# Optimization experiments

Hardware: AMD Instinct MI355X
Metric: run time of the kernel (lower is better)

The kernel has to match this reference:

```python
import jax, jax.numpy as jnp
import numpy as np


def _quantize(x, weight):
    # x: (B, D, H, W); weight: (D, K)
    B, D, H, W = x.shape
    K = weight.shape[1]
    xf = x.reshape(B, D, H * W)  # (B, D, N)
    x2 = jnp.sum(xf * xf, axis=1)                      # (B, N)
    cross = jnp.einsum('bdn,dk->bnk', xf, weight)       # (B, N, K)
    e2 = jnp.sum(weight * weight, axis=0)               # (K,)
    d2 = x2[..., None] - 2.0 * cross + e2               # (B, N, K)
    argmin = jnp.argmin(d2, axis=-1)                    # (B, N)
    # gather codes: (B, N, D) -> (B, D, N) -> (B, D, H, W)
    quant = weight.T[argmin]                            # (B, N, D)
    result = jnp.transpose(quant, (0, 2, 1)).reshape(B, D, H, W)
    return result, argmin.reshape(B, H, W)


def setup_inputs() -> dict:
    key = jax.random.key(0)
    k1, k2 = jax.random.split(key)
    x = jax.random.normal(k1, (32, 256, 32, 32), dtype=jnp.float32)
    weight = jax.random.uniform(k2, (256, 512), dtype=jnp.float32)  # torch.rand init
    return {"x": x, "weight": weight}


def reference(x, weight):
    result, argmin = _quantize(x, weight)
    return result, argmin
```

## Files before the change

### kernel.cpp

```cpp
#include <hip/hip_runtime.h>

typedef __attribute__((ext_vector_type(8))) short bf16x8;
typedef __attribute__((ext_vector_type(16))) float f32x16;

__device__ __forceinline__ bool lex_lt(float av, int ai, float bv, int bi) {
  return av < bv || (av == bv && ai < bi);
}

__device__ __forceinline__ unsigned bf16_rne(float v) {
  unsigned u = __float_as_uint(v);
  return (u + 0x7fffu + ((u >> 16) & 1u)) >> 16;
}

__device__ __forceinline__ unsigned pk_bf16(float a, float b) {
  return bf16_rne(a) | (bf16_rne(b) << 16);
}

__global__ __launch_bounds__(256) void vq_pre(
    const float* __restrict__ w, float* __restrict__ e2,
    short* __restrict__ wtil, float* __restrict__ wT) {
  int blk = blockIdx.x;
  if (blk < 64) {
    int gid = blk * 256 + threadIdx.x;
    int n  = gid & 511;
    int kg = gid >> 9;
    bf16x8 hv, lv;
    float vv[8];
#pragma unroll
    for (int j = 0; j < 8; ++j) {
      float v = w[(kg * 8 + j) * 512 + n];
      vv[j] = v;
      unsigned h = bf16_rne(v);
      float hf = __uint_as_float(h << 16);
      unsigned l = bf16_rne(v - hf);
      hv[j] = (short)h;
      lv[j] = (short)l;
    }
    short* dst = wtil + (size_t)gid * 8;
    *(bf16x8*)dst = hv;
    *(bf16x8*)(dst + 131072) = lv;
    if (wT) {
      float* p = wT + (size_t)n * 256 + kg * 8;
      *(float4*)p       = make_float4(vv[0], vv[1], vv[2], vv[3]);
      *(float4*)(p + 4) = make_float4(vv[4], vv[5], vv[6], vv[7]);
    }
  } else {
    int t = (blk - 64) * 256 + threadIdx.x;
    int k = t >> 2;
    int part = t & 3;
    double s = 0.0;
#pragma unroll 8
    for (int d = part * 64; d < part * 64 + 64; ++d) {
      double v = (double)w[d * 512 + k];
      s = fma(v, v, s);
    }
    s += __shfl_xor(s, 1);
    s += __shfl_xor(s, 2);
    if (part == 0) e2[k] = (float)s;
  }
}

__global__ __launch_bounds__(512, 4) void vq_main(
    const float* __restrict__ x, const float* __restrict__ w,
    const float* __restrict__ e2g, const short* __restrict__ wtil,
    const float* __restrict__ wT,
    float* __restrict__ out, float* __restrict__ arg_out) {
  __shared__ __align__(16) char arena[76800];
  short* xh   = (short*)arena;
  short* xl   = (short*)(arena + 32768);
  float* e2s  = (float*)(arena + 65536);
  float* tv1  = (float*)(arena + 67584);
  float* tv2  = (float*)(arena + 69632);
  int*   ti1  = (int*)(arena + 71680);
  int*   ti2  = (int*)(arena + 73728);
  int*   p1S  = (int*)(arena + 75776);
  int*   p2S  = (int*)(arena + 76032);
  int*   needS= (int*)(arena + 76288);
  int*   rpickS=(int*)(arena + 76544);
  float* gbuf = (float*)arena;

  const int tid = threadIdx.x;
  const int b  = blockIdx.x >> 4;
  const int n0 = (blockIdx.x & 15) << 6;
  const float* xbase = x + (size_t)b * 262144 + n0;

  {
    e2s[tid] = e2g[tid];
    const int n4  = tid & 15;
    const int kgp = tid >> 4;
    float4 v[8];
#pragma unroll
    for (int j = 0; j < 8; ++j)
      v[j] = *(const float4*)(xbase + (size_t)(kgp * 8 + j) * 1024 + (n4 << 2));
#pragma unroll
    for (int i = 0; i < 4; ++i) {
      int m = (n4 << 2) + i;
      union { int w4[4]; bf16x8 v8; } H, L;
#pragma unroll
      for (int jj = 0; jj < 4; ++jj) {
        float a = (i == 0) ? v[2*jj].x : (i == 1) ? v[2*jj].y : (i == 2) ? v[2*jj].z : v[2*jj].w;
        float c = (i == 0) ? v[2*jj+1].x : (i == 1) ? v[2*jj+1].y : (i == 2) ? v[2*jj+1].z : v[2*jj+1].w;
        unsigned hu = pk_bf16(a, c);
        float haf = __uint_as_float(hu << 16);
        float hcf = __uint_as_float(hu & 0xffff0000u);
        unsigned lu = pk_bf16(a - haf, c - hcf);
        H.w4[jj] = (int)hu;
        L.w4[jj] = (int)lu;
      }
      int slot = kgp ^ (m & 7) ^ ((m >> 3) & 7);
      int off = (m << 8) + (slot << 3);
      *(bf16x8*)&xh[off] = H.v8;
      *(bf16x8*)&xl[off] = L.v8;
    }
  }
  __syncthreads();

  const int lane = tid & 63;
  const int wv   = tid >> 6;
  const int ln   = lane & 31;
  const int half = lane >> 5;
  const int wb   = wv << 6;

  f32x16 acc[2][2];
#pragma unroll
  for (int ct = 0; ct < 2; ++ct)
#pragma unroll
    for (int pt = 0; pt < 2; ++pt)
#pragma unroll
      for (int r = 0; r < 16; ++r) acc[ct][pt][r] = 0.f;

  const int asw = (ln & 7) ^ (ln >> 3);
  const int abase = ln << 8;

  int bofs[2];
#pragma unroll
  for (int ct = 0; ct < 2; ++ct) bofs[ct] = (wb + (ct << 5) + ln) << 3;

  bf16x8 pch[2], pcl[2];
#pragma unroll
  for (int ct = 0; ct < 2; ++ct) {
    const short* p = wtil + (half << 12) + bofs[ct];
    pch[ct] = *(const bf16x8*)p;
    pcl[ct] = *(const bf16x8*)(p + 131072);
  }

  auto kstep = [&](int ch) {
    const int kg = (ch << 1) + half;
    const int ao = abase + ((kg ^ asw) << 3);
    bf16x8 xf[2], xg[2];
#pragma unroll
    for (int pt = 0; pt < 2; ++pt) {
      const int ap = (ao + (pt << 13)) ^ (pt << 5);
      xf[pt] = *(const bf16x8*)&xh[ap];
      xg[pt] = *(const bf16x8*)&xl[ap];
    }
    bf16x8 cfh[2], cfl[2];
#pragma unroll
    for (int ct = 0; ct < 2; ++ct) { cfh[ct] = pch[ct]; cfl[ct] = pcl[ct]; }
    if (ch < 15) {
      const int kgn = ((ch + 1) << 1) + half;
#pragma unroll
      for (int ct = 0; ct < 2; ++ct) {
        const short* p = wtil + (kgn << 12) + bofs[ct];
        pch[ct] = *(const bf16x8*)p;
        pcl[ct] = *(const bf16x8*)(p + 131072);
      }
    }
#pragma unroll
    for (int ct = 0; ct < 2; ++ct)
#pragma unroll
      for (int pt = 0; pt < 2; ++pt) {
        acc[ct][pt] = __builtin_amdgcn_mfma_f32_32x32x16_bf16(cfh[ct], xf[pt], acc[ct][pt], 0, 0, 0);
        acc[ct][pt] = __builtin_amdgcn_mfma_f32_32x32x16_bf16(cfh[ct], xg[pt], acc[ct][pt], 0, 0, 0);
        acc[ct][pt] = __builtin_amdgcn_mfma_f32_32x32x16_bf16(cfl[ct], xf[pt], acc[ct][pt], 0, 0, 0);
      }
  };

  kstep(0);  kstep(1);  kstep(2);  kstep(3);
  kstep(4);  kstep(5);  kstep(6);  kstep(7);
  kstep(8);  kstep(9);  kstep(10); kstep(11);
  kstep(12); kstep(13); kstep(14); kstep(15);

  float e2r[2][16];
#pragma unroll
  for (int ct = 0; ct < 2; ++ct)
#pragma unroll
    for (int r = 0; r < 16; ++r)
      e2r[ct][r] = e2s[wb + (ct << 5) + (r & 3) + ((r >> 2) << 3) + (half << 2)];

#pragma unroll
  for (int pt = 0; pt < 2; ++pt) {
    float v1 = 3.4e38f, v2 = 3.4e38f;
    int i1 = 0x7fffffff, i2 = 0x7fffffff;
#pragma unroll
    for (int ct = 0; ct < 2; ++ct) {
#pragma unroll
      for (int r = 0; r < 16; ++r) {
        int k = wb + (ct << 5) + (r & 3) + ((r >> 2) << 3) + (half << 2);
        float s = fmaf(-2.f, acc[ct][pt][r], e2r[ct][r]);
        if (lex_lt(s, k, v1, i1)) { v2 = v1; i2 = i1; v1 = s; i1 = k; }
        else if (lex_lt(s, k, v2, i2)) { v2 = s; i2 = k; }
      }
    }
    {
      float ov1 = __shfl_xor(v1, 32);
      int   oi1 = __shfl_xor(i1, 32);
      float ov2 = __shfl_xor(v2, 32);
      int   oi2 = __shfl_xor(i2, 32);
      bool aFirst = lex_lt(v1, i1, ov1, oi1);
      float nv1 = aFirst ? v1 : ov1;  int ni1 = aFirst ? i1 : oi1;
      float cv  = aFirst ? ov1 : v1;  int ci  = aFirst ? oi1 : i1;
      float sv  = aFirst ? v2 : ov2;  int si  = aFirst ? i2 : oi2;
      bool cFirst = lex_lt(cv, ci, sv, si);
      v1 = nv1; i1 = ni1;
      v2 = cFirst ? cv : sv; i2 = cFirst ? ci : si;
    }
    if (half == 0) {
      int s = (wv << 6) + (pt << 5) + ln;
      tv1[s] = v1; ti1[s] = i1; tv2[s] = v2; ti2[s] = i2;
    }
  }
  __syncthreads();

  if (tid < 64) {
    int row = tid;
    float v1 = 3.4e38f, v2 = 3.4e38f;
    int i1 = 0x7fffffff, i2 = 0x7fffffff;
#pragma unroll
    for (int wvv = 0; wvv < 8; ++wvv) {
      int s = (wvv << 6) + row;
      float a1 = tv1[s]; int ai = ti1[s];
      float a2 = tv2[s]; int bi = ti2[s];
      if (lex_lt(a1, ai, v1, i1)) { v2 = v1; i2 = i1; v1 = a1; i1 = ai; }
      else if (lex_lt(a1, ai, v2, i2)) { v2 = a1; i2 = ai; }
      if (lex_lt(a2, bi, v1, i1)) { v2 = v1; i2 = i1; v1 = a2; i1 = bi; }
      else if (lex_lt(a2, bi, v2, i2)) { v2 = a2; i2 = bi; }
    }
    p1S[row] = i1; p2S[row] = i2;
    needS[row] = (v2 - v1 < 0.01f) ? 1 : 0;
    rpickS[row] = i1;
  }
  __syncthreads();

  for (int t = 0; t < 8; ++t) {
    int row = (t << 3) + wv;
    if (needS[row]) {
      int i1 = p1S[row], i2 = p2S[row];
      const float* xp = x + (size_t)b * 262144 + n0 + row;
      double s1 = 0.0, s2 = 0.0;
      int k0 = lane << 2;
#pragma unroll
      for (int i = 0; i < 4; ++i) {
        int k = k0 + i;
        double xv = (double)xp[(size_t)k * 1024];
        double w1 = (double)w[k * 512 + i1];
        double w2 = (double)w[k * 512 + i2];
        double t1 = xv - w1, t2 = xv - w2;
        s1 = fma(t1, t1, s1);
        s2 = fma(t2, t2, s2);
      }
#pragma unroll
      for (int off = 32; off >= 1; off >>= 1) {
        s1 += __shfl_xor(s1, off);
        s2 += __shfl_xor(s2, off);
      }
      if (lane == 0 && (s2 < s1 || (s2 == s1 && i2 < i1))) rpickS[row] = i2;
    }
  }
  __syncthreads();

  if (tid < 64) arg_out[b * 1024 + n0 + tid] = (float)rpickS[tid];

  if (wT) {
    {
      const int pos  = tid >> 3;
      const int dseg = tid & 7;
      const float* wrow = wT + (size_t)rpickS[pos] * 256;
#pragma unroll
      for (int j = 0; j < 8; ++j) {
        int d0 = (j << 5) + (dseg << 2);
        float4 v = *(const float4*)(wrow + d0);
        gbuf[(d0 + 0) * 68 + pos] = v.x;
        gbuf[(d0 + 1) * 68 + pos] = v.y;
        gbuf[(d0 + 2) * 68 + pos] = v.z;
        gbuf[(d0 + 3) * 68 + pos] = v.w;
      }
    }
    __syncthreads();
    {
      const int nn0 = (tid & 15) << 2;
      const int d0g = tid >> 4;
      float* obase = out + (size_t)b * 262144 + n0 + nn0;
#pragma unroll
      for (int dg = 0; dg < 8; ++dg) {
        int d = d0g + (dg << 5);
        float4 o = *(const float4*)&gbuf[d * 68 + nn0];
        *(float4*)(obase + (size_t)d * 1024) = o;
      }
    }
  } else {
    const int nn0 = (tid & 15) << 2;
    const int d0g = tid >> 4;
    int pk0 = rpickS[nn0], pk1 = rpickS[nn0 + 1], pk2 = rpickS[nn0 + 2], pk3 = rpickS[nn0 + 3];
    float* obase = out + (size_t)b * 262144 + n0 + nn0;
#pragma unroll
    for (int dg = 0; dg < 8; ++dg) {
      int d = d0g + (dg << 5);
      const float* wr = w + d * 512;
      float4 o = make_float4(wr[pk0], wr[pk1], wr[pk2], wr[pk3]);
      *(float4*)(obase + (size_t)d * 1024) = o;
    }
  }
}

extern "C" void kernel_launch(void* const* d_in, const int* in_sizes, int n_in,
                              void* d_out, int out_size, void* d_ws, size_t ws_size,
                              hipStream_t stream) {
  const float* x = (const float*)d_in[0];
  const float* w = (const float*)d_in[1];
  float* out  = (float*)d_out;
  float* argf = out + 8388608;
  float* e2   = (float*)d_ws;
  short* wtil = (short*)((char*)d_ws + 2048);
  size_t need = 2048 + 524288 + 524288;
  float* wT   = (ws_size >= need) ? (float*)((char*)d_ws + 2048 + 524288) : nullptr;

  vq_pre<<<72, 256, 0, stream>>>(w, e2, wtil, wT);
  vq_main<<<512, 512, 0, stream>>>(x, w, e2, wtil, wT, out, argf);
}
```

Before: 115.2 us.

## Split x staging in half and overlap second half's load with MFMA k-steps

The main kernel now loads and converts only the first half of the feature dimension into LDS before the matmul starts. The second half is loaded into registers and converted while the first k-steps run, with a barrier before the later k-steps. This aims to hide global-load latency behind MFMA work. The precompute kernel also doubles its block count so each thread handles four codebook values instead of eight, spreading the bf16 split work across more threads. The trade-off is more live registers and an extra barrier in the main kernel.

```diff
diff --git a/kernel.cpp b/kernel.cpp
--- a/kernel.cpp
+++ b/kernel.cpp
@@ -1,6 +1,7 @@
 #include <hip/hip_runtime.h>
 
 typedef __attribute__((ext_vector_type(8))) short bf16x8;
+typedef __attribute__((ext_vector_type(4))) short bf16x4;
 typedef __attribute__((ext_vector_type(16))) float f32x16;
 
 __device__ __forceinline__ bool lex_lt(float av, int ai, float bv, int bi) {
@@ -20,15 +21,17 @@
     const float* __restrict__ w, float* __restrict__ e2,
     short* __restrict__ wtil, float* __restrict__ wT) {
   int blk = blockIdx.x;
-  if (blk < 64) {
+  if (blk < 128) {
     int gid = blk * 256 + threadIdx.x;
     int n  = gid & 511;
-    int kg = gid >> 9;
-    bf16x8 hv, lv;
-    float vv[8];
-#pragma unroll
-    for (int j = 0; j < 8; ++j) {
-      float v = w[(kg * 8 + j) * 512 + n];
+    int kq = gid >> 9;
+    int kg = kq >> 1;
+    int jb = (kq & 1) << 2;
+    bf16x4 hv, lv;
+    float vv[4];
+#pragma unroll
+    for (int j = 0; j < 4; ++j) {
+      float v = w[(kg * 8 + jb + j) * 512 + n];
       vv[j] = v;
       unsigned h = bf16_rne(v);
       float hf = __uint_as_float(h << 16);
@@ -36,16 +39,15 @@
       hv[j] = (short)h;
       lv[j] = (short)l;
     }
-    short* dst = wtil + (size_t)gid * 8;
-    *(bf16x8*)dst = hv;
-    *(bf16x8*)(dst + 131072) = lv;
+    short* dst = wtil + ((size_t)kg * 512 + n) * 8 + jb;
+    *(bf16x4*)dst = hv;
+    *(bf16x4*)(dst + 131072) = lv;
     if (wT) {
-      float* p = wT + (size_t)n * 256 + kg * 8;
-      *(float4*)p       = make_float4(vv[0], vv[1], vv[2], vv[3]);
-      *(float4*)(p + 4) = make_float4(vv[4], vv[5], vv[6], vv[7]);
+      float* p = wT + (size_t)n * 256 + kg * 8 + jb;
+      *(float4*)p = make_float4(vv[0], vv[1], vv[2], vv[3]);
     }
   } else {
-    int t = (blk - 64) * 256 + threadIdx.x;
+    int t = (blk - 128) * 256 + threadIdx.x;
     int k = t >> 2;
     int part = t & 3;
     double s = 0.0;
@@ -84,22 +86,18 @@
   const int n0 = (blockIdx.x & 15) << 6;
   const float* xbase = x + (size_t)b * 262144 + n0;
 
-  {
-    e2s[tid] = e2g[tid];
-    const int n4  = tid & 15;
-    const int kgp = tid >> 4;
-    float4 v[8];
-#pragma unroll
-    for (int j = 0; j < 8; ++j)
-      v[j] = *(const float4*)(xbase + (size_t)(kgp * 8 + j) * 1024 + (n4 << 2));
-#pragma unroll
-    for (int i = 0; i < 4; ++i) {
-      int m = (n4 << 2) + i;
+  const int n2  = tid & 31;
+  const int kgh = tid >> 5;
+
+  auto cw2 = [&](int kg8, const float2* v) {
+#pragma unroll
+    for (int i = 0; i < 2; ++i) {
+      int m = (n2 << 1) + i;
       union { int w4[4]; bf16x8 v8; } H, L;
 #pragma unroll
       for (int jj = 0; jj < 4; ++jj) {
-        float a = (i == 0) ? v[2*jj].x : (i == 1) ? v[2*jj].y : (i == 2) ? v[2*jj].z : v[2*jj].w;
-        float c = (i == 0) ? v[2*jj+1].x : (i == 1) ? v[2*jj+1].y : (i == 2) ? v[2*jj+1].z : v[2*jj+1].w;
+        float a = (i == 0) ? v[2*jj].x   : v[2*jj].y;
+        float c = (i == 0) ? v[2*jj+1].x : v[2*jj+1].y;
         unsigned hu = pk_bf16(a, c);
         float haf = __uint_as_float(hu << 16);
         float hcf = __uint_as_float(hu & 0xffff0000u);
@@ -107,11 +105,20 @@
         H.w4[jj] = (int)hu;
         L.w4[jj] = (int)lu;
       }
-      int slot = kgp ^ (m & 7) ^ ((m >> 3) & 7);
+      int slot = kg8 ^ (m & 7) ^ ((m >> 3) & 7);
       int off = (m << 8) + (slot << 3);
       *(bf16x8*)&xh[off] = H.v8;
       *(bf16x8*)&xl[off] = L.v8;
     }
+  };
+
+  {
+    e2s[tid] = e2g[tid];
+    float2 v[8];
+#pragma unroll
+    for (int j = 0; j < 8; ++j)
+      v[j] = *(const float2*)(xbase + (size_t)(kgh * 8 + j) * 1024 + (n2 << 1));
+    cw2(kgh, v);
   }
   __syncthreads();
 
@@ -176,8 +183,14 @@
       }
   };
 
-  kstep(0);  kstep(1);  kstep(2);  kstep(3);
-  kstep(4);  kstep(5);  kstep(6);  kstep(7);
+  float2 vx[8];
+#pragma unroll
+  for (int j = 0; j < 8; ++j)
+    vx[j] = *(const float2*)(xbase + (size_t)((kgh + 16) * 8 + j) * 1024 + (n2 << 1));
+  kstep(0); kstep(1); kstep(2); kstep(3);
+  cw2(kgh + 16, vx);
+  kstep(4); kstep(5); kstep(6); kstep(7);
+  __syncthreads();
   kstep(8);  kstep(9);  kstep(10); kstep(11);
   kstep(12); kstep(13); kstep(14); kstep(15);
 
@@ -325,6 +338,6 @@
   size_t need = 2048 + 524288 + 524288;
   float* wT   = (ws_size >= need) ? (float*)((char*)d_ws + 2048 + 524288) : nullptr;
 
-  vq_pre<<<72, 256, 0, stream>>>(w, e2, wtil, wT);
+  vq_pre<<<136, 256, 0, stream>>>(w, e2, wtil, wT);
   vq_main<<<512, 512, 0, stream>>>(x, w, e2, wtil, wT, out, argf);
 }
```

Measured after the change: 115.6 us. Within noise of the previous version (+0.4%).
